# Optimization experiments

Hardware: AMD Instinct MI355X
Metric: run time of the kernel (lower is better)

Reference implementation:

```python
import jax, jax.numpy as jnp
import numpy as np

B, T, D, H, E = 4, 2048, 1024, 1024, 8
NEG_SLOPE = 0.01  # torch LeakyReLU default

def leaky_relu(x):
    return jnp.where(x >= 0, x, NEG_SLOPE * x)

def setup_inputs() -> dict:
    key = jax.random.key(0)
    ks = jax.random.split(key, 10)
    s = 0.02
    return {
        "x": jax.random.normal(ks[0], (B, T, D), jnp.float32),
        "gate_w": jax.random.normal(ks[1], (D, E), jnp.float32) * s,
        "gate_b": jnp.zeros((E,), jnp.float32),
        "w1": jax.random.normal(ks[2], (E, D, H), jnp.float32) * s,
        "b1": jnp.zeros((E, H), jnp.float32),
        "w2": jax.random.normal(ks[3], (E, H, H), jnp.float32) * s,
        "b2": jnp.zeros((E, H), jnp.float32),
        "w3": jax.random.normal(ks[4], (E, H, D), jnp.float32) * s,
        "b3": jnp.zeros((E, D), jnp.float32),
        "topn": 2,
    }

def reference(x, gate_w, gate_b, w1, b1, w2, b2, w3, b3, topn):
    # Gating: softmax over experts, top-k mask, L1 renormalize
    gating = jax.nn.softmax(x @ gate_w + gate_b, axis=-1)          # [B,T,E]
    _, topk_idx = jax.lax.top_k(gating, topn)                       # [B,T,k]
    mask = jax.nn.one_hot(topk_idx, E, dtype=gating.dtype).sum(-2)  # [B,T,E]
    g = gating * mask
    g = g / jnp.maximum(jnp.sum(jnp.abs(g), axis=-1, keepdims=True), 1e-12)
    # Dense all-expert MLP: Linear -> LeakyReLU -> Linear -> LeakyReLU -> Linear
    h = leaky_relu(jnp.einsum('btd,edh->bteh', x, w1) + b1)         # [B,T,E,H]
    h = leaky_relu(jnp.einsum('bteh,ehg->bteg', h, w2) + b2)        # [B,T,E,H]
    eo = jnp.einsum('bteh,ehd->bted', h, w3) + b3                   # [B,T,E,D]
    # Weighted combine
    return jnp.einsum('bte,bted->btd', g, eo)                       # [B,T,D]
```

## Files before the change

### kernel.cpp

```cpp
#include <hip/hip_runtime.h>
#include <hip/hip_bf16.h>
#include <stdint.h>

#define TOKENS   8192
#define DDIM     1024
#define EXPERTS  8
#define NSLOT    (TOKENS * 2)
#define MAXTILE  136

typedef __bf16 bf16x8_t __attribute__((ext_vector_type(8)));
typedef __bf16 bf16x4_t __attribute__((ext_vector_type(4)));
typedef float  f32x4_t  __attribute__((ext_vector_type(4)));

__device__ __forceinline__ void gl_lds16(const void* g, void* l) {
  __builtin_amdgcn_global_load_lds(
      (const __attribute__((address_space(1))) void*)g,
      (__attribute__((address_space(3))) void*)l, 16, 0, 0);
}

__global__ void twt_k(const float* __restrict__ w1, const float* __restrict__ w2,
                      const float* __restrict__ w3, __bf16* __restrict__ w1T,
                      __bf16* __restrict__ w2T, __bf16* __restrict__ w3T) {
  __shared__ float tile[64][33];
  const int layer = blockIdx.z >> 3, e = blockIdx.z & 7;
  const float* w = (layer == 0) ? w1 : (layer == 1) ? w2 : w3;
  __bf16* wT = (layer == 0) ? w1T : (layer == 1) ? w2T : w3T;
  const int kb = blockIdx.x * 64, nb = blockIdx.y * 32;
  const size_t ebase = (size_t)e << 20;
  const int tx = threadIdx.x, ty = threadIdx.y;
  const float* src = w + ebase;
#pragma unroll
  for (int r = ty; r < 64; r += 8)
    tile[r][tx] = src[(size_t)(kb + r) * 1024 + nb + tx];
  __syncthreads();
  __bf16* dst = wT + ebase;
#pragma unroll
  for (int r = ty; r < 32; r += 8) {
    union { __bf16 h[2]; unsigned u; } pk;
    pk.h[0] = (__bf16)tile[2 * tx][r];
    pk.h[1] = (__bf16)tile[2 * tx + 1][r];
    *(unsigned*)(dst + (size_t)(nb + r) * 1024 + kb + 2 * tx) = pk.u;
  }
}

__global__ __launch_bounds__(256) void gate_k(
    const float* __restrict__ x, const float* __restrict__ gw,
    const float* __restrict__ gb, __bf16* __restrict__ xbf,
    int* __restrict__ top_i, float* __restrict__ top_w) {
  const int t = blockIdx.x * 4 + (threadIdx.x >> 6);
  const int lane = threadIdx.x & 63;
  const float4* x4 = (const float4*)(x + (size_t)t * DDIM);
  bf16x4_t* xo4 = (bf16x4_t*)(xbf + (size_t)t * DDIM);
  const float4* g4 = (const float4*)gw;
  float acc[EXPERTS];
#pragma unroll
  for (int e = 0; e < EXPERTS; ++e) acc[e] = 0.f;
#pragma unroll
  for (int d4 = lane; d4 < 256; d4 += 64) {
    const float4 v = x4[d4];
    bf16x4_t o = {(__bf16)v.x, (__bf16)v.y, (__bf16)v.z, (__bf16)v.w};
    xo4[d4] = o;
    const float4* g = g4 + (size_t)d4 * 8;
    float4 ga, gbv;
    ga = g[0]; gbv = g[1];
    acc[0] += v.x * ga.x; acc[1] += v.x * ga.y; acc[2] += v.x * ga.z; acc[3] += v.x * ga.w;
    acc[4] += v.x * gbv.x; acc[5] += v.x * gbv.y; acc[6] += v.x * gbv.z; acc[7] += v.x * gbv.w;
    ga = g[2]; gbv = g[3];
    acc[0] += v.y * ga.x; acc[1] += v.y * ga.y; acc[2] += v.y * ga.z; acc[3] += v.y * ga.w;
    acc[4] += v.y * gbv.x; acc[5] += v.y * gbv.y; acc[6] += v.y * gbv.z; acc[7] += v.y * gbv.w;
    ga = g[4]; gbv = g[5];
    acc[0] += v.z * ga.x; acc[1] += v.z * ga.y; acc[2] += v.z * ga.z; acc[3] += v.z * ga.w;
    acc[4] += v.z * gbv.x; acc[5] += v.z * gbv.y; acc[6] += v.z * gbv.z; acc[7] += v.z * gbv.w;
    ga = g[6]; gbv = g[7];
    acc[0] += v.w * ga.x; acc[1] += v.w * ga.y; acc[2] += v.w * ga.z; acc[3] += v.w * ga.w;
    acc[4] += v.w * gbv.x; acc[5] += v.w * gbv.y; acc[6] += v.w * gbv.z; acc[7] += v.w * gbv.w;
  }
#pragma unroll
  for (int e = 0; e < EXPERTS; ++e)
    for (int s = 32; s > 0; s >>= 1) acc[e] += __shfl_down(acc[e], s);
  if (lane == 0) {
#pragma unroll
    for (int e = 0; e < EXPERTS; ++e) acc[e] += gb[e];
    int i1 = 0;
    for (int e = 1; e < EXPERTS; ++e)
      if (acc[e] > acc[i1]) i1 = e;
    int i2 = (i1 == 0) ? 1 : 0;
    for (int e = 0; e < EXPERTS; ++e)
      if (e != i1 && acc[e] > acc[i2]) i2 = e;
    const float r = expf(acc[i2] - acc[i1]);
    const float wA = 1.f / (1.f + r);
    const float wB = r / (1.f + r);
    top_i[t * 2] = i1; top_i[t * 2 + 1] = i2;
    top_w[t * 2] = wA; top_w[t * 2 + 1] = wB;
  }
}

__global__ __launch_bounds__(1024) void plan_k(
    const int* __restrict__ top_i, int* __restrict__ eoff,
    int* __restrict__ tok_list, int* __restrict__ slot_of,
    int* __restrict__ work, int* __restrict__ ntiles) {
  const int tid = threadIdx.x;
  const int lane = tid & 63, wid = tid >> 6;
  __shared__ int ws[16][EXPERTS];
  __shared__ int eoff_s[EXPERTS];
  __shared__ int base_lds[1024 * EXPERTS];

  int ids[16];
  unsigned long long h64 = 0;
#pragma unroll
  for (int j = 0; j < 16; ++j) {
    ids[j] = top_i[tid * 16 + j];
    h64 += 1ull << (ids[j] * 8);
  }
#pragma unroll
  for (int e = 0; e < EXPERTS; ++e) {
    const int h = (int)((h64 >> (8 * e)) & 0xff);
    int v = h;
    for (int s = 1; s < 64; s <<= 1) {
      const int u = __shfl_up(v, s);
      if (lane >= s) v += u;
    }
    const int excl = v - h;
    const int tot = __shfl(v, 63);
    if (lane == 0) ws[wid][e] = tot;
    base_lds[tid * EXPERTS + e] = excl;
  }
  __syncthreads();
  if (tid == 0) {
    int tot[EXPERTS];
    for (int e = 0; e < EXPERTS; ++e) {
      int run = 0;
      for (int w = 0; w < 16; ++w) { const int c = ws[w][e]; ws[w][e] = run; run += c; }
      tot[e] = run;
    }
    int s = 0, nt = 0;
    for (int e = 0; e < EXPERTS; ++e) {
      eoff_s[e] = s; eoff[e] = s; s += tot[e];
      const int mt = (tot[e] + 127) >> 7;
      for (int i = 0; i < mt; ++i) work[nt++] = (e << 16) | i;
    }
    eoff[EXPERTS] = s;
    ntiles[0] = nt;
  }
  __syncthreads();
#pragma unroll
  for (int e = 0; e < EXPERTS; ++e)
    base_lds[tid * EXPERTS + e] += eoff_s[e] + ws[wid][e];
  unsigned long long pre64 = 0;
#pragma unroll
  for (int j = 0; j < 16; ++j) {
    const int entry = tid * 16 + j;
    const int e = ids[j];
    const int pre = (int)((pre64 >> (8 * e)) & 0xff);
    pre64 += 1ull << (8 * e);
    const int s = base_lds[tid * EXPERTS + e] + pre;
    tok_list[s] = entry >> 1;
    slot_of[entry] = s;
  }
}

template <int GATHER, int LEAKY>
__global__ __launch_bounds__(256) void moe_gemm(
    const __bf16* __restrict__ A, const int* __restrict__ tok,
    const __bf16* __restrict__ W, const float* __restrict__ bias,
    const int* __restrict__ eoff, const int* __restrict__ work,
    const int* __restrict__ ntiles, __bf16* __restrict__ out) {
  if ((int)blockIdx.y >= ntiles[0]) return;
  const int wk = work[blockIdx.y];
  const int e = wk >> 16;
  const int m0 = (wk & 0xffff) * 128;
  const int off = eoff[e];
  const int ne = eoff[e + 1] - off;
  const int n0 = blockIdx.x * 128;

  __shared__ __align__(16) __bf16 As[128 * 32];
  __shared__ __align__(16) __bf16 Bs[128 * 32];

  const int tid = threadIdx.x;
  const int lane = tid & 63;
  const int wid = tid >> 6;
  const int wm = wid >> 1, wn = wid & 1;
  const int ln = lane & 15, quad = lane >> 4;

  const __bf16* aptr[2];
  const __bf16* bptr[2];
  __bf16* alds[2];
  __bf16* blds[2];
#pragma unroll
  for (int j = 0; j < 2; ++j) {
    const int c = (wid * 2 + j) * 64 + lane;
    const int row = c >> 2;
    const int kc = (c & 3) ^ ((row >> 1) & 3);
    int r = m0 + row;
    if (r >= ne) r = m0;
    const long arow = GATHER ? (long)tok[off + r] : (long)(off + r);
    aptr[j] = A + arow * DDIM + kc * 8;
    alds[j] = (__bf16*)As + (wid * 2 + j) * 512;
    bptr[j] = W + ((long)e << 20) + (long)(n0 + row) * 1024 + kc * 8;
    blds[j] = (__bf16*)Bs + (wid * 2 + j) * 512;
  }

  const int swz = (quad ^ ((ln >> 1) & 3)) * 8;

  const f32x4_t vzero = {0.f, 0.f, 0.f, 0.f};
  f32x4_t acc[4][4];
#pragma unroll
  for (int i = 0; i < 4; ++i)
#pragma unroll
    for (int j = 0; j < 4; ++j) acc[i][j] = vzero;

  for (int kt = 0; kt < 32; ++kt) {
    const int k0 = kt * 32;
    __syncthreads();
    gl_lds16(aptr[0] + k0, alds[0]);
    gl_lds16(aptr[1] + k0, alds[1]);
    gl_lds16(bptr[0] + k0, blds[0]);
    gl_lds16(bptr[1] + k0, blds[1]);
    __syncthreads();

    bf16x8_t aF[4], bF[4];
#pragma unroll
    for (int i = 0; i < 4; ++i)
      aF[i] = *(const bf16x8_t*)(As + (wm * 64 + i * 16 + ln) * 32 + swz);
#pragma unroll
    for (int j = 0; j < 4; ++j)
      bF[j] = *(const bf16x8_t*)(Bs + (wn * 64 + j * 16 + ln) * 32 + swz);
#pragma unroll
    for (int i = 0; i < 4; ++i)
#pragma unroll
      for (int j = 0; j < 4; ++j)
        acc[i][j] = __builtin_amdgcn_mfma_f32_16x16x32_bf16(aF[i], bF[j],
                                                            acc[i][j], 0, 0, 0);
  }

  const float* bs = bias + e * 1024;
#pragma unroll
  for (int i = 0; i < 4; ++i) {
    const int rloc = wm * 64 + i * 16 + quad * 4;
#pragma unroll
    for (int j = 0; j < 4; ++j) {
      const int col = n0 + wn * 64 + j * 16 + ln;
      const float bv = bs[col];
#pragma unroll
      for (int r = 0; r < 4; ++r) {
        const int m = m0 + rloc + r;
        if (m < ne) {
          float v = acc[i][j][r] + bv;
          if (LEAKY) v = (v >= 0.f) ? v : 0.01f * v;
          out[(size_t)(off + m) * 1024 + col] = (__bf16)v;
        }
      }
    }
  }
}

__global__ __launch_bounds__(256) void combine_k(
    const __bf16* __restrict__ eo, const int* __restrict__ slot_of,
    const float* __restrict__ top_w, float* __restrict__ out) {
  const int t = blockIdx.x;
  const int s1 = slot_of[t * 2], s2 = slot_of[t * 2 + 1];
  const float w1 = top_w[t * 2], w2 = top_w[t * 2 + 1];
  const bf16x4_t a = ((const bf16x4_t*)(eo + (size_t)s1 * DDIM))[threadIdx.x];
  const bf16x4_t b = ((const bf16x4_t*)(eo + (size_t)s2 * DDIM))[threadIdx.x];
  float4 o;
  o.x = w1 * (float)a[0] + w2 * (float)b[0];
  o.y = w1 * (float)a[1] + w2 * (float)b[1];
  o.z = w1 * (float)a[2] + w2 * (float)b[2];
  o.w = w1 * (float)a[3] + w2 * (float)b[3];
  ((float4*)(out + (size_t)t * DDIM))[threadIdx.x] = o;
}

extern "C" void kernel_launch(void* const* d_in, const int* in_sizes, int n_in,
                              void* d_out, int out_size, void* d_ws,
                              size_t ws_size, hipStream_t stream) {
  (void)in_sizes; (void)n_in; (void)out_size; (void)ws_size;
  const float* x  = (const float*)d_in[0];
  const float* gw = (const float*)d_in[1];
  const float* gb = (const float*)d_in[2];
  const float* w1 = (const float*)d_in[3];
  const float* b1 = (const float*)d_in[4];
  const float* w2 = (const float*)d_in[5];
  const float* b2 = (const float*)d_in[6];
  const float* w3 = (const float*)d_in[7];
  const float* b3 = (const float*)d_in[8];
  float* out = (float*)d_out;

  uint8_t* p = (uint8_t*)d_ws;
  auto alloc = [&](size_t b) {
    uint8_t* r = p;
    p += (b + 255) & ~(size_t)255;
    return r;
  };
  int*    eoff     = (int*)alloc(4 * (EXPERTS + 1));
  int*    ntiles   = (int*)alloc(4);
  int*    work     = (int*)alloc(4 * MAXTILE);
  int*    top_i    = (int*)alloc(4ull * TOKENS * 2);
  float*  top_w    = (float*)alloc(4ull * TOKENS * 2);
  int*    slot_of  = (int*)alloc(4ull * TOKENS * 2);
  int*    tok_list = (int*)alloc(4ull * NSLOT);
  __bf16* xbf      = (__bf16*)alloc(2ull * TOKENS * DDIM);
  __bf16* w1T      = (__bf16*)alloc(2ull * EXPERTS * 1024 * 1024);
  __bf16* w2T      = (__bf16*)alloc(2ull * EXPERTS * 1024 * 1024);
  __bf16* w3T      = (__bf16*)alloc(2ull * EXPERTS * 1024 * 1024);
  __bf16* h1       = (__bf16*)alloc(2ull * NSLOT * 1024);
  __bf16* h2       = (__bf16*)alloc(2ull * NSLOT * 1024);
  __bf16* eo       = (__bf16*)alloc(2ull * NSLOT * 1024);

  gate_k<<<TOKENS / 4, 256, 0, stream>>>(x, gw, gb, xbf, top_i, top_w);
  twt_k<<<dim3(16, 32, 24), dim3(32, 8), 0, stream>>>(w1, w2, w3, w1T, w2T, w3T);
  plan_k<<<1, 1024, 0, stream>>>(top_i, eoff, tok_list, slot_of, work, ntiles);

  moe_gemm<1, 1><<<dim3(8, MAXTILE), 256, 0, stream>>>(
      xbf, tok_list, w1T, b1, eoff, work, ntiles, h1);
  moe_gemm<0, 1><<<dim3(8, MAXTILE), 256, 0, stream>>>(
      h1, tok_list, w2T, b2, eoff, work, ntiles, h2);
  moe_gemm<0, 0><<<dim3(8, MAXTILE), 256, 0, stream>>>(
      h2, tok_list, w3T, b3, eoff, work, ntiles, eo);

  combine_k<<<TOKENS, 256, 0, stream>>>(eo, slot_of, top_w, out);
}
```

Before: 434.2 us.

## Triple-buffer LDS loads in MoE GEMM and vectorize transposed epilogue stores

The expert GEMM now uses a three-stage LDS ring with direct global-to-LDS loads issued two K-steps ahead, synchronized by vmcnt waits plus one barrier per step instead of two. This is meant to hide global load latency behind MFMA work. The MFMA operands are swapped so each lane holds four consecutive columns, which lets the epilogue write packed 4-wide bf16 stores and load bias as float4. Work items now carry expert, row offset, base and count directly, removing the eoff lookups. The cost is three times the LDS and a dependence on exact vmcnt accounting.

```diff
diff --git a/kernel.cpp b/kernel.cpp
--- a/kernel.cpp
+++ b/kernel.cpp
@@ -98,7 +98,7 @@
 __global__ __launch_bounds__(1024) void plan_k(
     const int* __restrict__ top_i, int* __restrict__ eoff,
     int* __restrict__ tok_list, int* __restrict__ slot_of,
-    int* __restrict__ work, int* __restrict__ ntiles) {
+    int4* __restrict__ work, int* __restrict__ ntiles) {
   const int tid = threadIdx.x;
   const int lane = tid & 63, wid = tid >> 6;
   __shared__ int ws[16][EXPERTS];
@@ -135,9 +135,11 @@
     }
     int s = 0, nt = 0;
     for (int e = 0; e < EXPERTS; ++e) {
-      eoff_s[e] = s; eoff[e] = s; s += tot[e];
-      const int mt = (tot[e] + 127) >> 7;
-      for (int i = 0; i < mt; ++i) work[nt++] = (e << 16) | i;
+      const int te = tot[e];
+      eoff_s[e] = s; eoff[e] = s;
+      const int mt = (te + 127) >> 7;
+      for (int i = 0; i < mt; ++i) { work[nt] = make_int4(e, i << 7, s, te); ++nt; }
+      s += te;
     }
     eoff[EXPERTS] = s;
     ntiles[0] = nt;
@@ -163,18 +165,18 @@
 __global__ __launch_bounds__(256) void moe_gemm(
     const __bf16* __restrict__ A, const int* __restrict__ tok,
     const __bf16* __restrict__ W, const float* __restrict__ bias,
-    const int* __restrict__ eoff, const int* __restrict__ work,
-    const int* __restrict__ ntiles, __bf16* __restrict__ out) {
+    const int4* __restrict__ work, const int* __restrict__ ntiles,
+    __bf16* __restrict__ out) {
   if ((int)blockIdx.y >= ntiles[0]) return;
-  const int wk = work[blockIdx.y];
-  const int e = wk >> 16;
-  const int m0 = (wk & 0xffff) * 128;
-  const int off = eoff[e];
-  const int ne = eoff[e + 1] - off;
+  const int4 wk = work[blockIdx.y];
+  const int e = wk.x;
+  const int m0 = wk.y;
+  const int off = wk.z;
+  const int ne = wk.w;
   const int n0 = blockIdx.x * 128;
 
-  __shared__ __align__(16) __bf16 As[128 * 32];
-  __shared__ __align__(16) __bf16 Bs[128 * 32];
+  __shared__ __align__(16) __bf16 As[3][128 * 32];
+  __shared__ __align__(16) __bf16 Bs[3][128 * 32];
 
   const int tid = threadIdx.x;
   const int lane = tid & 63;
@@ -184,8 +186,6 @@
 
   const __bf16* aptr[2];
   const __bf16* bptr[2];
-  __bf16* alds[2];
-  __bf16* blds[2];
 #pragma unroll
   for (int j = 0; j < 2; ++j) {
     const int c = (wid * 2 + j) * 64 + lane;
@@ -195,10 +195,10 @@
     if (r >= ne) r = m0;
     const long arow = GATHER ? (long)tok[off + r] : (long)(off + r);
     aptr[j] = A + arow * DDIM + kc * 8;
-    alds[j] = (__bf16*)As + (wid * 2 + j) * 512;
     bptr[j] = W + ((long)e << 20) + (long)(n0 + row) * 1024 + kc * 8;
-    blds[j] = (__bf16*)Bs + (wid * 2 + j) * 512;
-  }
+  }
+  const int st0 = (wid * 2) * 512;
+  const int st1 = (wid * 2 + 1) * 512;
 
   const int swz = (quad ^ ((ln >> 1) & 3)) * 8;
 
@@ -209,46 +209,76 @@
 #pragma unroll
     for (int j = 0; j < 4; ++j) acc[i][j] = vzero;
 
-  for (int kt = 0; kt < 32; ++kt) {
-    const int k0 = kt * 32;
-    __syncthreads();
-    gl_lds16(aptr[0] + k0, alds[0]);
-    gl_lds16(aptr[1] + k0, alds[1]);
-    gl_lds16(bptr[0] + k0, blds[0]);
-    gl_lds16(bptr[1] + k0, blds[1]);
-    __syncthreads();
-
-    bf16x8_t aF[4], bF[4];
-#pragma unroll
-    for (int i = 0; i < 4; ++i)
-      aF[i] = *(const bf16x8_t*)(As + (wm * 64 + i * 16 + ln) * 32 + swz);
-#pragma unroll
-    for (int j = 0; j < 4; ++j)
-      bF[j] = *(const bf16x8_t*)(Bs + (wn * 64 + j * 16 + ln) * 32 + swz);
-#pragma unroll
-    for (int i = 0; i < 4; ++i)
-#pragma unroll
-      for (int j = 0; j < 4; ++j)
-        acc[i][j] = __builtin_amdgcn_mfma_f32_16x16x32_bf16(aF[i], bF[j],
-                                                            acc[i][j], 0, 0, 0);
-  }
-
-  const float* bs = bias + e * 1024;
+#define STAGE(SB, KT)                                        \
+  do {                                                       \
+    const int k0_ = (KT) * 32;                               \
+    gl_lds16(aptr[0] + k0_, (__bf16*)As[SB] + st0);          \
+    gl_lds16(aptr[1] + k0_, (__bf16*)As[SB] + st1);          \
+    gl_lds16(bptr[0] + k0_, (__bf16*)Bs[SB] + st0);          \
+    gl_lds16(bptr[1] + k0_, (__bf16*)Bs[SB] + st1);          \
+  } while (0)
+
+#define WAITB(N)                                             \
+  do {                                                       \
+    asm volatile("s_waitcnt vmcnt(" #N ")" ::: "memory");    \
+    __builtin_amdgcn_s_barrier();                            \
+  } while (0)
+
+#define COMPUTE(CUR)                                                        \
+  do {                                                                      \
+    bf16x8_t aF[4], bF[4];                                                  \
+    _Pragma("unroll") for (int i = 0; i < 4; ++i)                           \
+        aF[i] = *(const bf16x8_t*)(&As[CUR][(wm * 64 + i * 16 + ln) * 32 +  \
+                                            swz]);                          \
+    _Pragma("unroll") for (int j = 0; j < 4; ++j)                           \
+        bF[j] = *(const bf16x8_t*)(&Bs[CUR][(wn * 64 + j * 16 + ln) * 32 +  \
+                                            swz]);                          \
+    _Pragma("unroll") for (int i = 0; i < 4; ++i)                           \
+        _Pragma("unroll") for (int j = 0; j < 4; ++j)                       \
+            acc[i][j] = __builtin_amdgcn_mfma_f32_16x16x32_bf16(            \
+                bF[j], aF[i], acc[i][j], 0, 0, 0);                          \
+  } while (0)
+
+  STAGE(0, 0);
+  STAGE(1, 1);
+
+#pragma unroll 1
+  for (int kt = 0; kt < 30; kt += 3) {
+    WAITB(4); STAGE(2, kt + 2); COMPUTE(0);
+    WAITB(4); STAGE(0, kt + 3); COMPUTE(1);
+    WAITB(4); STAGE(1, kt + 4); COMPUTE(2);
+  }
+  WAITB(4); COMPUTE(0);
+  WAITB(0); COMPUTE(1);
+
+#undef STAGE
+#undef WAITB
+#undef COMPUTE
+
+  const float* bs = bias + (e << 10);
+  const int nb = n0 + wn * 64 + quad * 4;
+  float4 bv[4];
+#pragma unroll
+  for (int j = 0; j < 4; ++j) bv[j] = *(const float4*)(bs + nb + j * 16);
 #pragma unroll
   for (int i = 0; i < 4; ++i) {
-    const int rloc = wm * 64 + i * 16 + quad * 4;
-#pragma unroll
-    for (int j = 0; j < 4; ++j) {
-      const int col = n0 + wn * 64 + j * 16 + ln;
-      const float bv = bs[col];
-#pragma unroll
-      for (int r = 0; r < 4; ++r) {
-        const int m = m0 + rloc + r;
-        if (m < ne) {
-          float v = acc[i][j][r] + bv;
-          if (LEAKY) v = (v >= 0.f) ? v : 0.01f * v;
-          out[(size_t)(off + m) * 1024 + col] = (__bf16)v;
+    const int m = m0 + wm * 64 + i * 16 + ln;
+    if (m < ne) {
+      __bf16* orow = out + (size_t)(off + m) * 1024 + nb;
+#pragma unroll
+      for (int j = 0; j < 4; ++j) {
+        float t0 = acc[i][j][0] + bv[j].x;
+        float t1 = acc[i][j][1] + bv[j].y;
+        float t2 = acc[i][j][2] + bv[j].z;
+        float t3 = acc[i][j][3] + bv[j].w;
+        if (LEAKY) {
+          t0 = (t0 >= 0.f) ? t0 : 0.01f * t0;
+          t1 = (t1 >= 0.f) ? t1 : 0.01f * t1;
+          t2 = (t2 >= 0.f) ? t2 : 0.01f * t2;
+          t3 = (t3 >= 0.f) ? t3 : 0.01f * t3;
         }
+        bf16x4_t pk = {(__bf16)t0, (__bf16)t1, (__bf16)t2, (__bf16)t3};
+        *(bf16x4_t*)(orow + j * 16) = pk;
       }
     }
   }
@@ -293,7 +323,7 @@
   };
   int*    eoff     = (int*)alloc(4 * (EXPERTS + 1));
   int*    ntiles   = (int*)alloc(4);
-  int*    work     = (int*)alloc(4 * MAXTILE);
+  int4*   work     = (int4*)alloc(16 * MAXTILE);
   int*    top_i    = (int*)alloc(4ull * TOKENS * 2);
   float*  top_w    = (float*)alloc(4ull * TOKENS * 2);
   int*    slot_of  = (int*)alloc(4ull * TOKENS * 2);
@@ -311,11 +341,11 @@
   plan_k<<<1, 1024, 0, stream>>>(top_i, eoff, tok_list, slot_of, work, ntiles);
 
   moe_gemm<1, 1><<<dim3(8, MAXTILE), 256, 0, stream>>>(
-      xbf, tok_list, w1T, b1, eoff, work, ntiles, h1);
+      xbf, tok_list, w1T, b1, work, ntiles, h1);
   moe_gemm<0, 1><<<dim3(8, MAXTILE), 256, 0, stream>>>(
-      h1, tok_list, w2T, b2, eoff, work, ntiles, h2);
+      h1, tok_list, w2T, b2, work, ntiles, h2);
   moe_gemm<0, 0><<<dim3(8, MAXTILE), 256, 0, stream>>>(
-      h2, tok_list, w3T, b3, eoff, work, ntiles, eo);
+      h2, tok_list, w3T, b3, work, ntiles, eo);
 
   combine_k<<<TOKENS, 256, 0, stream>>>(eo, slot_of, top_w, out);
 }
```

Result: slower. 462.2 us (+6.4%).
